# Performance work log

Hardware: AMD Instinct MI355X
Metric: run time of the kernel (lower is better)

Reference implementation:

```python
import jax, jax.numpy as jnp
import numpy as np
import math

N_NODES = 100000
N_EDGES = 1600000
D_FEAT = 32
K = 1        # Bernstein index k
N_ORD = 2    # Bernstein order n
COMB = float(math.comb(N_ORD, K))


def setup_inputs() -> dict:
    key = jax.random.key(0)
    k1, k2, k3 = jax.random.split(key, 3)
    feat = jax.random.normal(k1, (N_NODES, D_FEAT), dtype=jnp.float32)
    edge_src = jax.random.randint(k2, (N_EDGES,), 0, N_NODES)
    edge_dst = jax.random.randint(k3, (N_EDGES,), 0, N_NODES)
    return {"feat": feat, "edge_src": edge_src, "edge_dst": edge_dst}


def reference(feat, edge_src, edge_dst):
    # in-degree of each node (copy_u/sum aggregates over incoming edges)
    deg = jax.ops.segment_sum(jnp.ones((N_EDGES,), feat.dtype), edge_dst,
                              num_segments=N_NODES)
    d_invsqrt = jnp.clip(deg, 1.0, None) ** -0.5  # [N]
    d_invsqrt = d_invsqrt[:, None]                 # [N,1]

    def unn_laplacian(x):
        msg = (x * d_invsqrt)[edge_src]            # [E,D]
        agg = jax.ops.segment_sum(msg, edge_dst, num_segments=N_NODES)
        return x - agg * d_invsqrt

    if K == 0:
        h = feat
        for _ in range(N_ORD):
            h = unn_laplacian(h) / 2
            h = feat - h
    elif K == N_ORD:
        h = feat
        for _ in range(N_ORD):
            h = unn_laplacian(h) / 2
    else:
        temp = feat
        for _ in range(K):
            temp = unn_laplacian(temp) / 2
        h = feat
        for _ in range(N_ORD - K):
            h = unn_laplacian(h) / 2
            h = feat - h
        h = temp * h
    return COMB * h
```

## Files before the change

### kernel.cpp

```cpp
#include <hip/hip_runtime.h>

#define N_NODES 100000
#define N_EDGES 1600000
#define D_FEAT 32

#define BSH 7
#define BMASK 127
#define NB 782
#define CAPB 2432

#define P1_BS 1024
#define P1_TILE 8192
#define P1_CAP 16


typedef float v4f __attribute__((ext_vector_type(4)));

static __device__ __forceinline__ unsigned pack_bf16(float a, float b) {
    unsigned ua = __float_as_uint(a);
    unsigned ub = __float_as_uint(b);
    ua = (ua + 0x7FFFu + ((ua >> 16) & 1u)) >> 16;
    ub = (ub + 0x7FFFu + ((ub >> 16) & 1u)) >> 16;
    return (ua & 0xFFFFu) | (ub << 16);
}

__global__ void init_kernel(int* __restrict__ cursorA) {
    int b = blockIdx.x * blockDim.x + threadIdx.x;
    if (b < NB) cursorA[b] = b * CAPB;
}

__global__ void __launch_bounds__(P1_BS)
bucket_kernel(const int* __restrict__ edge_src,
              const int* __restrict__ edge_dst,
              int* __restrict__ cursorA,
              int* __restrict__ pairs, int n_edges) {
    __shared__ int s_cnt[NB];
    __shared__ int s_base[NB];
    __shared__ int s_buf[NB * P1_CAP];

    int tile = blockIdx.x * P1_TILE;
    if (tile >= n_edges) return;

    for (int b = threadIdx.x; b < NB; b += P1_BS) s_cnt[b] = 0;
    __syncthreads();

    const int4* src4 = reinterpret_cast<const int4*>(edge_src);
    const int4* dst4 = reinterpret_cast<const int4*>(edge_dst);
    int tileq = blockIdx.x * (P1_TILE / 4);
    #pragma unroll
    for (int j = 0; j < 2; ++j) {
        int iq = tileq + j * P1_BS + threadIdx.x;
        if (iq * 4 < n_edges) {
            int4 sv = src4[iq];
            int4 dv = dst4[iq];
            int ss[4] = {sv.x, sv.y, sv.z, sv.w};
            int dd[4] = {dv.x, dv.y, dv.z, dv.w};
            #pragma unroll
            for (int u = 0; u < 4; ++u) {
                int b = dd[u] >> BSH;
                int packed = (ss[u] << BSH) | (dd[u] & BMASK);
                int p = atomicAdd(&s_cnt[b], 1);
                if (p < P1_CAP) {
                    s_buf[b * P1_CAP + p] = packed;
                } else {
                    int gp = atomicAdd(&cursorA[b], 1);
                    pairs[gp] = packed;
                }
            }
        }
    }
    __syncthreads();

    for (int b = threadIdx.x; b < NB; b += P1_BS) {
        int c = min(s_cnt[b], P1_CAP);
        s_cnt[b] = c;
        s_base[b] = atomicAdd(&cursorA[b], c);
    }
    __syncthreads();

    for (int idx = threadIdx.x; idx < NB * P1_CAP; idx += P1_BS) {
        int b = idx >> 4;
        int slot = idx & (P1_CAP - 1);
        if (slot < s_cnt[b])
            pairs[s_base[b] + slot] = s_buf[idx];
    }
}

__global__ void __launch_bounds__(512)
prep_kernel(const int* __restrict__ pairs,
            const int* __restrict__ cursorA,
            const float* __restrict__ feat,
            unsigned* __restrict__ sfeat) {
    __shared__ int h[128];
    __shared__ float dv_s[128];

    int b = blockIdx.x;
    int t = threadIdx.x;
    int base = b * CAPB;
    int cnt = min(cursorA[b] - base, CAPB);

    if (t < 128) h[t] = 0;
    __syncthreads();
    for (int i = t; i < cnt; i += 512)
        atomicAdd(&h[pairs[base + i] & BMASK], 1);
    __syncthreads();

    if (t < 128)
        dv_s[t] = rsqrtf(fmaxf((float)h[t], 1.0f));
    __syncthreads();

    const float4* feat4 = reinterpret_cast<const float4*>(feat);
    uint4* sf4 = reinterpret_cast<uint4*>(sfeat);
    for (int idx = t; idx < 128 * 4; idx += 512) {
        int nl = idx >> 2;
        int q = idx & 3;
        int node = (b << BSH) + nl;
        if (node >= N_NODES) continue;
        float dvv = dv_s[nl];
        float4 fa = feat4[node * 8 + 2 * q];
        float4 fb = feat4[node * 8 + 2 * q + 1];
        uint4 pk;
        pk.x = pack_bf16(fa.x * dvv, fa.y * dvv);
        pk.y = pack_bf16(fa.z * dvv, fa.w * dvv);
        pk.z = pack_bf16(fb.x * dvv, fb.y * dvv);
        pk.w = pack_bf16(fb.z * dvv, fb.w * dvv);
        sf4[node * 4 + q] = pk;
    }
}

__global__ void __launch_bounds__(512)
sortgather_kernel(const int* __restrict__ pairs,
                  const int* __restrict__ cursorA,
                  const float* __restrict__ feat,
                  const unsigned* __restrict__ sfeat,
                  float* __restrict__ out) {
    __shared__ int buf[CAPB];
    __shared__ int outb[CAPB];
    __shared__ int h[128];
    __shared__ int sc[128];
    __shared__ int cur[128];
    __shared__ float dv_s[128];

    int b = blockIdx.x;
    int t = threadIdx.x;
    int base = b * CAPB;
    int cnt = min(cursorA[b] - base, CAPB);

    if (t < 128) h[t] = 0;
    __syncthreads();
    for (int i = t; i < cnt; i += 512) {
        int p = pairs[base + i];
        buf[i] = p;
        atomicAdd(&h[p & BMASK], 1);
    }
    __syncthreads();

    if (t < 64) {
        int a  = h[2 * t];
        int b2 = h[2 * t + 1];
        int s = a + b2;
        #pragma unroll
        for (int off = 1; off < 64; off <<= 1) {
            int x = __shfl_up(s, off);
            if (t >= off) s += x;
        }
        sc[2 * t]     = s - b2;
        sc[2 * t + 1] = s;
    }
    __syncthreads();
    if (t < 128) {
        cur[t] = sc[t] - h[t];
        dv_s[t] = rsqrtf(fmaxf((float)h[t], 1.0f));
    }
    __syncthreads();

    for (int i = t; i < cnt; i += 512) {
        int p = buf[i];
        int pos = atomicAdd(&cur[p & BMASK], 1);
        outb[pos] = p >> BSH;
    }
    __syncthreads();

    const uint4* sf4 = reinterpret_cast<const uint4*>(sfeat);
    const v4f* featv = reinterpret_cast<const v4f*>(feat);
    v4f* outv = reinterpret_cast<v4f*>(out);

    {
        int nl = t >> 2;
        int q = t & 3;
        int node = (b << BSH) + nl;
        if (node < N_NODES) {
            int en = sc[nl];
            int k = en - h[nl];
            float a0 = 0.f, a1 = 0.f, a2 = 0.f, a3 = 0.f;
            float a4 = 0.f, a5 = 0.f, a6 = 0.f, a7 = 0.f;

            #define ACC(r)                                                 \
                a0 += __uint_as_float((r).x << 16);                        \
                a1 += __uint_as_float((r).x & 0xFFFF0000u);                \
                a2 += __uint_as_float((r).y << 16);                        \
                a3 += __uint_as_float((r).y & 0xFFFF0000u);                \
                a4 += __uint_as_float((r).z << 16);                        \
                a5 += __uint_as_float((r).z & 0xFFFF0000u);                \
                a6 += __uint_as_float((r).w << 16);                        \
                a7 += __uint_as_float((r).w & 0xFFFF0000u);

            for (; k + 7 < en; k += 8) {
                int s0 = outb[k],     s1 = outb[k + 1];
                int s2 = outb[k + 2], s3 = outb[k + 3];
                int s4 = outb[k + 4], s5 = outb[k + 5];
                int s6 = outb[k + 6], s7 = outb[k + 7];
                uint4 r0 = sf4[s0 * 4 + q];
                uint4 r1 = sf4[s1 * 4 + q];
                uint4 r2 = sf4[s2 * 4 + q];
                uint4 r3 = sf4[s3 * 4 + q];
                uint4 r4 = sf4[s4 * 4 + q];
                uint4 r5 = sf4[s5 * 4 + q];
                uint4 r6 = sf4[s6 * 4 + q];
                uint4 r7 = sf4[s7 * 4 + q];
                ACC(r0) ACC(r1) ACC(r2) ACC(r3)
                ACC(r4) ACC(r5) ACC(r6) ACC(r7)
            }
            for (; k + 3 < en; k += 4) {
                int s0 = outb[k],     s1 = outb[k + 1];
                int s2 = outb[k + 2], s3 = outb[k + 3];
                uint4 r0 = sf4[s0 * 4 + q];
                uint4 r1 = sf4[s1 * 4 + q];
                uint4 r2 = sf4[s2 * 4 + q];
                uint4 r3 = sf4[s3 * 4 + q];
                ACC(r0) ACC(r1) ACC(r2) ACC(r3)
            }
            for (; k < en; ++k) {
                uint4 r = sf4[outb[k] * 4 + q];
                ACC(r)
            }
            #undef ACC

            float dvn = dv_s[nl];
            v4f fa = __builtin_nontemporal_load(&featv[node * 8 + 2 * q]);
            v4f fb = __builtin_nontemporal_load(&featv[node * 8 + 2 * q + 1]);
            v4f oa, ob;
            float y;
            y = 0.5f * (fa.x - a0 * dvn); oa.x = 2.0f * y * (fa.x - y);
            y = 0.5f * (fa.y - a1 * dvn); oa.y = 2.0f * y * (fa.y - y);
            y = 0.5f * (fa.z - a2 * dvn); oa.z = 2.0f * y * (fa.z - y);
            y = 0.5f * (fa.w - a3 * dvn); oa.w = 2.0f * y * (fa.w - y);
            y = 0.5f * (fb.x - a4 * dvn); ob.x = 2.0f * y * (fb.x - y);
            y = 0.5f * (fb.y - a5 * dvn); ob.y = 2.0f * y * (fb.y - y);
            y = 0.5f * (fb.z - a6 * dvn); ob.z = 2.0f * y * (fb.z - y);
            y = 0.5f * (fb.w - a7 * dvn); ob.w = 2.0f * y * (fb.w - y);
            __builtin_nontemporal_store(oa, &outv[node * 8 + 2 * q]);
            __builtin_nontemporal_store(ob, &outv[node * 8 + 2 * q + 1]);
        }
    }
}

extern "C" void kernel_launch(void* const* d_in, const int* in_sizes, int n_in,
                              void* d_out, int out_size, void* d_ws, size_t ws_size,
                              hipStream_t stream) {
    const float* feat = (const float*)d_in[0];
    const int* edge_src = (const int*)d_in[1];
    const int* edge_dst = (const int*)d_in[2];
    float* out = (float*)d_out;

    int* ws = (int*)d_ws;
    int* cursorA    = ws;
    int* pairs      = cursorA + 1024;
    unsigned* sfeat = (unsigned*)(pairs + NB * CAPB);

    init_kernel<<<1, 1024, 0, stream>>>(cursorA);
    {
        int blocks = (N_EDGES + P1_TILE - 1) / P1_TILE;
        bucket_kernel<<<blocks, P1_BS, 0, stream>>>(edge_src, edge_dst,
                                                    cursorA, pairs, N_EDGES);
    }
    prep_kernel<<<NB, 512, 0, stream>>>(pairs, cursorA, feat, sfeat);
    sortgather_kernel<<<NB, 512, 0, stream>>>(pairs, cursorA, feat, sfeat, out);
}
```

Measured before the change: 113.5 us.

## Move per-bucket histogram and scan into prep kernel and share ranges

```diff
diff --git a/kernel.cpp b/kernel.cpp
--- a/kernel.cpp
+++ b/kernel.cpp
@@ -22,11 +22,6 @@
     ua = (ua + 0x7FFFu + ((ua >> 16) & 1u)) >> 16;
     ub = (ub + 0x7FFFu + ((ub >> 16) & 1u)) >> 16;
     return (ua & 0xFFFFu) | (ub << 16);
-}
-
-__global__ void init_kernel(int* __restrict__ cursorA) {
-    int b = blockIdx.x * blockDim.x + threadIdx.x;
-    if (b < NB) cursorA[b] = b * CAPB;
 }
 
 __global__ void __launch_bounds__(P1_BS)
@@ -64,7 +59,7 @@
                     s_buf[b * P1_CAP + p] = packed;
                 } else {
                     int gp = atomicAdd(&cursorA[b], 1);
-                    pairs[gp] = packed;
+                    if (gp < CAPB) pairs[b * CAPB + gp] = packed;
                 }
             }
         }
@@ -74,7 +69,7 @@
     for (int b = threadIdx.x; b < NB; b += P1_BS) {
         int c = min(s_cnt[b], P1_CAP);
         s_cnt[b] = c;
-        s_base[b] = atomicAdd(&cursorA[b], c);
+        s_base[b] = b * CAPB + atomicAdd(&cursorA[b], c);
     }
     __syncthreads();
 
@@ -90,14 +85,17 @@
 prep_kernel(const int* __restrict__ pairs,
             const int* __restrict__ cursorA,
             const float* __restrict__ feat,
+            int2* __restrict__ srange,
+            float* __restrict__ dinv,
             unsigned* __restrict__ sfeat) {
     __shared__ int h[128];
+    __shared__ int sc[128];
     __shared__ float dv_s[128];
 
     int b = blockIdx.x;
     int t = threadIdx.x;
     int base = b * CAPB;
-    int cnt = min(cursorA[b] - base, CAPB);
+    int cnt = min(cursorA[b], CAPB);
 
     if (t < 128) h[t] = 0;
     __syncthreads();
@@ -105,8 +103,29 @@
         atomicAdd(&h[pairs[base + i] & BMASK], 1);
     __syncthreads();
 
-    if (t < 128)
-        dv_s[t] = rsqrtf(fmaxf((float)h[t], 1.0f));
+    if (t < 64) {
+        int a  = h[2 * t];
+        int b2 = h[2 * t + 1];
+        int s = a + b2;
+        #pragma unroll
+        for (int off = 1; off < 64; off <<= 1) {
+            int x = __shfl_up(s, off);
+            if (t >= off) s += x;
+        }
+        sc[2 * t]     = s - b2;
+        sc[2 * t + 1] = s;
+    }
+    __syncthreads();
+    if (t < 128) {
+        int node = (b << BSH) + t;
+        if (node < N_NODES) {
+            int v = h[t];
+            srange[node] = make_int2(base + sc[t] - v, base + sc[t]);
+            float dvv = rsqrtf(fmaxf((float)v, 1.0f));
+            dinv[node] = dvv;
+            dv_s[t] = dvv;
+        }
+    }
     __syncthreads();
 
     const float4* feat4 = reinterpret_cast<const float4*>(feat);
@@ -131,51 +150,32 @@
 __global__ void __launch_bounds__(512)
 sortgather_kernel(const int* __restrict__ pairs,
                   const int* __restrict__ cursorA,
+                  const int2* __restrict__ srange,
+                  const float* __restrict__ dinv,
                   const float* __restrict__ feat,
                   const unsigned* __restrict__ sfeat,
                   float* __restrict__ out) {
-    __shared__ int buf[CAPB];
     __shared__ int outb[CAPB];
-    __shared__ int h[128];
-    __shared__ int sc[128];
+    __shared__ int st[128];
+    __shared__ int en[128];
     __shared__ int cur[128];
-    __shared__ float dv_s[128];
 
     int b = blockIdx.x;
     int t = threadIdx.x;
     int base = b * CAPB;
-    int cnt = min(cursorA[b] - base, CAPB);
-
-    if (t < 128) h[t] = 0;
-    __syncthreads();
+    int cnt = min(cursorA[b], CAPB);
+
+    if (t < 128) {
+        int node = (b << BSH) + t;
+        int2 se = (node < N_NODES) ? srange[node] : make_int2(base, base);
+        st[t] = se.x - base;
+        en[t] = se.y - base;
+        cur[t] = se.x - base;
+    }
+    __syncthreads();
+
     for (int i = t; i < cnt; i += 512) {
         int p = pairs[base + i];
-        buf[i] = p;
-        atomicAdd(&h[p & BMASK], 1);
-    }
-    __syncthreads();
-
-    if (t < 64) {
-        int a  = h[2 * t];
-        int b2 = h[2 * t + 1];
-        int s = a + b2;
-        #pragma unroll
-        for (int off = 1; off < 64; off <<= 1) {
-            int x = __shfl_up(s, off);
-            if (t >= off) s += x;
-        }
-        sc[2 * t]     = s - b2;
-        sc[2 * t + 1] = s;
-    }
-    __syncthreads();
-    if (t < 128) {
-        cur[t] = sc[t] - h[t];
-        dv_s[t] = rsqrtf(fmaxf((float)h[t], 1.0f));
-    }
-    __syncthreads();
-
-    for (int i = t; i < cnt; i += 512) {
-        int p = buf[i];
         int pos = atomicAdd(&cur[p & BMASK], 1);
         outb[pos] = p >> BSH;
     }
@@ -185,73 +185,71 @@
     const v4f* featv = reinterpret_cast<const v4f*>(feat);
     v4f* outv = reinterpret_cast<v4f*>(out);
 
-    {
-        int nl = t >> 2;
-        int q = t & 3;
-        int node = (b << BSH) + nl;
-        if (node < N_NODES) {
-            int en = sc[nl];
-            int k = en - h[nl];
-            float a0 = 0.f, a1 = 0.f, a2 = 0.f, a3 = 0.f;
-            float a4 = 0.f, a5 = 0.f, a6 = 0.f, a7 = 0.f;
-
-            #define ACC(r)                                                 \
-                a0 += __uint_as_float((r).x << 16);                        \
-                a1 += __uint_as_float((r).x & 0xFFFF0000u);                \
-                a2 += __uint_as_float((r).y << 16);                        \
-                a3 += __uint_as_float((r).y & 0xFFFF0000u);                \
-                a4 += __uint_as_float((r).z << 16);                        \
-                a5 += __uint_as_float((r).z & 0xFFFF0000u);                \
-                a6 += __uint_as_float((r).w << 16);                        \
-                a7 += __uint_as_float((r).w & 0xFFFF0000u);
-
-            for (; k + 7 < en; k += 8) {
-                int s0 = outb[k],     s1 = outb[k + 1];
-                int s2 = outb[k + 2], s3 = outb[k + 3];
-                int s4 = outb[k + 4], s5 = outb[k + 5];
-                int s6 = outb[k + 6], s7 = outb[k + 7];
-                uint4 r0 = sf4[s0 * 4 + q];
-                uint4 r1 = sf4[s1 * 4 + q];
-                uint4 r2 = sf4[s2 * 4 + q];
-                uint4 r3 = sf4[s3 * 4 + q];
-                uint4 r4 = sf4[s4 * 4 + q];
-                uint4 r5 = sf4[s5 * 4 + q];
-                uint4 r6 = sf4[s6 * 4 + q];
-                uint4 r7 = sf4[s7 * 4 + q];
-                ACC(r0) ACC(r1) ACC(r2) ACC(r3)
-                ACC(r4) ACC(r5) ACC(r6) ACC(r7)
-            }
-            for (; k + 3 < en; k += 4) {
-                int s0 = outb[k],     s1 = outb[k + 1];
-                int s2 = outb[k + 2], s3 = outb[k + 3];
-                uint4 r0 = sf4[s0 * 4 + q];
-                uint4 r1 = sf4[s1 * 4 + q];
-                uint4 r2 = sf4[s2 * 4 + q];
-                uint4 r3 = sf4[s3 * 4 + q];
-                ACC(r0) ACC(r1) ACC(r2) ACC(r3)
-            }
-            for (; k < en; ++k) {
-                uint4 r = sf4[outb[k] * 4 + q];
-                ACC(r)
-            }
-            #undef ACC
-
-            float dvn = dv_s[nl];
-            v4f fa = __builtin_nontemporal_load(&featv[node * 8 + 2 * q]);
-            v4f fb = __builtin_nontemporal_load(&featv[node * 8 + 2 * q + 1]);
-            v4f oa, ob;
-            float y;
-            y = 0.5f * (fa.x - a0 * dvn); oa.x = 2.0f * y * (fa.x - y);
-            y = 0.5f * (fa.y - a1 * dvn); oa.y = 2.0f * y * (fa.y - y);
-            y = 0.5f * (fa.z - a2 * dvn); oa.z = 2.0f * y * (fa.z - y);
-            y = 0.5f * (fa.w - a3 * dvn); oa.w = 2.0f * y * (fa.w - y);
-            y = 0.5f * (fb.x - a4 * dvn); ob.x = 2.0f * y * (fb.x - y);
-            y = 0.5f * (fb.y - a5 * dvn); ob.y = 2.0f * y * (fb.y - y);
-            y = 0.5f * (fb.z - a6 * dvn); ob.z = 2.0f * y * (fb.z - y);
-            y = 0.5f * (fb.w - a7 * dvn); ob.w = 2.0f * y * (fb.w - y);
-            __builtin_nontemporal_store(oa, &outv[node * 8 + 2 * q]);
-            __builtin_nontemporal_store(ob, &outv[node * 8 + 2 * q + 1]);
-        }
+    int nl = t >> 2;
+    int q = t & 3;
+    int node = (b << BSH) + nl;
+    if (node < N_NODES) {
+        int k = st[nl];
+        int e = en[nl];
+        float a0 = 0.f, a1 = 0.f, a2 = 0.f, a3 = 0.f;
+        float a4 = 0.f, a5 = 0.f, a6 = 0.f, a7 = 0.f;
+
+        #define ACC(r)                                                 \
+            a0 += __uint_as_float((r).x << 16);                        \
+            a1 += __uint_as_float((r).x & 0xFFFF0000u);                \
+            a2 += __uint_as_float((r).y << 16);                        \
+            a3 += __uint_as_float((r).y & 0xFFFF0000u);                \
+            a4 += __uint_as_float((r).z << 16);                        \
+            a5 += __uint_as_float((r).z & 0xFFFF0000u);                \
+            a6 += __uint_as_float((r).w << 16);                        \
+            a7 += __uint_as_float((r).w & 0xFFFF0000u);
+
+        for (; k + 7 < e; k += 8) {
+            int s0 = outb[k],     s1 = outb[k + 1];
+            int s2 = outb[k + 2], s3 = outb[k + 3];
+            int s4 = outb[k + 4], s5 = outb[k + 5];
+            int s6 = outb[k + 6], s7 = outb[k + 7];
+            uint4 r0 = sf4[s0 * 4 + q];
+            uint4 r1 = sf4[s1 * 4 + q];
+            uint4 r2 = sf4[s2 * 4 + q];
+            uint4 r3 = sf4[s3 * 4 + q];
+            uint4 r4 = sf4[s4 * 4 + q];
+            uint4 r5 = sf4[s5 * 4 + q];
+            uint4 r6 = sf4[s6 * 4 + q];
+            uint4 r7 = sf4[s7 * 4 + q];
+            ACC(r0) ACC(r1) ACC(r2) ACC(r3)
+            ACC(r4) ACC(r5) ACC(r6) ACC(r7)
+        }
+        for (; k + 3 < e; k += 4) {
+            int s0 = outb[k],     s1 = outb[k + 1];
+            int s2 = outb[k + 2], s3 = outb[k + 3];
+            uint4 r0 = sf4[s0 * 4 + q];
+            uint4 r1 = sf4[s1 * 4 + q];
+            uint4 r2 = sf4[s2 * 4 + q];
+            uint4 r3 = sf4[s3 * 4 + q];
+            ACC(r0) ACC(r1) ACC(r2) ACC(r3)
+        }
+        for (; k < e; ++k) {
+            uint4 r = sf4[outb[k] * 4 + q];
+            ACC(r)
+        }
+        #undef ACC
+
+        float dvn = dinv[node];
+        v4f fa = __builtin_nontemporal_load(&featv[node * 8 + 2 * q]);
+        v4f fb = __builtin_nontemporal_load(&featv[node * 8 + 2 * q + 1]);
+        v4f oa, ob;
+        float y;
+        y = 0.5f * (fa.x - a0 * dvn); oa.x = 2.0f * y * (fa.x - y);
+        y = 0.5f * (fa.y - a1 * dvn); oa.y = 2.0f * y * (fa.y - y);
+        y = 0.5f * (fa.z - a2 * dvn); oa.z = 2.0f * y * (fa.z - y);
+        y = 0.5f * (fa.w - a3 * dvn); oa.w = 2.0f * y * (fa.w - y);
+        y = 0.5f * (fb.x - a4 * dvn); ob.x = 2.0f * y * (fb.x - y);
+        y = 0.5f * (fb.y - a5 * dvn); ob.y = 2.0f * y * (fb.y - y);
+        y = 0.5f * (fb.z - a6 * dvn); ob.z = 2.0f * y * (fb.z - y);
+        y = 0.5f * (fb.w - a7 * dvn); ob.w = 2.0f * y * (fb.w - y);
+        __builtin_nontemporal_store(oa, &outv[node * 8 + 2 * q]);
+        __builtin_nontemporal_store(ob, &outv[node * 8 + 2 * q + 1]);
     }
 }
 
@@ -265,15 +263,18 @@
 
     int* ws = (int*)d_ws;
     int* cursorA    = ws;
-    int* pairs      = cursorA + 1024;
+    int2* srange    = (int2*)(cursorA + 1024);
+    float* dinv     = (float*)(srange + N_NODES);
+    int* pairs      = (int*)(dinv + N_NODES);
     unsigned* sfeat = (unsigned*)(pairs + NB * CAPB);
 
-    init_kernel<<<1, 1024, 0, stream>>>(cursorA);
+    hipMemsetAsync(cursorA, 0, 1024 * sizeof(int), stream);
     {
         int blocks = (N_EDGES + P1_TILE - 1) / P1_TILE;
         bucket_kernel<<<blocks, P1_BS, 0, stream>>>(edge_src, edge_dst,
                                                     cursorA, pairs, N_EDGES);
     }
-    prep_kernel<<<NB, 512, 0, stream>>>(pairs, cursorA, feat, sfeat);
-    sortgather_kernel<<<NB, 512, 0, stream>>>(pairs, cursorA, feat, sfeat, out);
-}
+    prep_kernel<<<NB, 512, 0, stream>>>(pairs, cursorA, feat, srange, dinv, sfeat);
+    sortgather_kernel<<<NB, 512, 0, stream>>>(pairs, cursorA, srange, dinv,
+                                              feat, sfeat, out);
+}
```

After: 114.4 us. About the same (+0.8%).
